# Performance work log

Measured on AMD Instinct MI355X. Metric: run time of the kernel, lower is better.

## Reference

```python
import jax, jax.numpy as jnp
import numpy as np

K1, K2 = 3, 3
DIL = 1
PAD = (DIL * (K1 - 1) // 2, DIL * (K2 - 1) // 2)


def _unfold(x, k1, k2, dilation, padding):
    # x: [B, C, H, W] -> patches [B, C, k1*k2, H*W], matching F.unfold ordering
    B, C, H, W = x.shape
    p0, p1 = padding
    xp = jnp.pad(x, ((0, 0), (0, 0), (p0, p0), (p1, p1)))
    cols = []
    for i in range(k1):  # small fixed loop over kernel taps
        for j in range(k2):
            cols.append(xp[:, :, i * dilation:i * dilation + H, j * dilation:j * dilation + W])
    patches = jnp.stack(cols, axis=2)  # [B, C, k1*k2, H, W]
    return patches.reshape(B, C, k1 * k2, H * W)


def setup_inputs() -> dict:
    key = jax.random.key(0)
    k1, k2, k3, k4 = jax.random.split(key, 4)
    B, Cin, Cout, H, W = 32, 128, 128, 32, 32
    x = jax.random.normal(k1, (B, Cin, H, W), dtype=jnp.float32)
    mask = jax.random.uniform(k2, (1, K1 * K2, H * W), dtype=jnp.float32)
    weight = jax.random.normal(k3, (Cout, Cin, K1, K2), dtype=jnp.float32) * 0.05
    bias = jax.random.normal(k4, (Cout,), dtype=jnp.float32) * 0.05
    return {"x": x, "mask": mask, "weight": weight, "bias": bias}


def reference(x, mask, weight, bias):
    B, Cin, H, W = x.shape
    Cout = weight.shape[0]
    KK = K1 * K2
    # unfold -> [B, Cin, KK, L]
    patches = _unfold(x, K1, K2, DIL, PAD)
    # per-patch mask multiply (mask broadcasts over B and Cin): mask [1, KK, L]
    patches = patches * mask[:, None, :, :]  # [B, Cin, KK, L]
    # dense matmul with flattened weight [Cout, Cin*KK]
    wm = weight.reshape(Cout, Cin * KK)
    out = jnp.einsum('ok,bkl->bol', wm, patches.reshape(B, Cin * KK, H * W))
    out = out + bias[None, :, None]
    return out.reshape(B, Cout, H, W)
```

## Files before the change

kernel.cpp:

```cpp
#include <hip/hip_runtime.h>
#include <hip/hip_fp16.h>

typedef _Float16 half8 __attribute__((ext_vector_type(8)));
typedef float f32x4 __attribute__((ext_vector_type(4)));

#define CIN   128
#define COUT  128
#define HH    32
#define WW    32
#define LTOT  1024
#define KKT   9
#define KDIM  1152

#define SMEM_BYTES 69632

__global__ void prep_w_kernel(const float* __restrict__ w, _Float16* __restrict__ wt) {
  int i = blockIdx.x * 256 + threadIdx.x;
  int q = i >> 10;
  int o = (i >> 3) & 127;
  int j = i & 7;
  int kk = q >> 4;
  int c  = ((q & 15) << 3) + j;
  wt[i] = (_Float16)w[(o * CIN + c) * KKT + kk];
}

__global__ __launch_bounds__(512, 2)
void conv_mfma_kernel(const float* __restrict__ x,
                      const _Float16* __restrict__ wt,
                      const float* __restrict__ mask,
                      const float* __restrict__ bias,
                      float* __restrict__ out) {
  extern __shared__ char smem[];
  const int tid = threadIdx.x;
  int bid = blockIdx.x;
  bid = (bid & 7) * 32 + (bid >> 3);
  const int b  = bid >> 3;
  const int l0 = (bid & 7) << 7;
  const int h0 = (bid & 7) << 2;

  const int lane = tid & 63, wid = tid >> 6;
  const int lr = lane & 15, lg = lane >> 4;
  const int kh = wid >> 2;
  const int wq = wid & 3;
  const int mw = (wq >> 1) << 6;
  const int nw = (wq & 1) << 6;

  float mv[9][4];
  {
    const float* mr = mask + l0 + nw + lr;
#pragma unroll
    for (int kk = 0; kk < 9; ++kk)
#pragma unroll
      for (int nj = 0; nj < 4; ++nj)
        mv[kk][nj] = mr[kk * LTOT + nj * 16];
  }

  const int wv = tid & 31, q16 = tid >> 5;
  char* bdst = smem + wv * 256 + ((q16 ^ (wv & 15)) << 4);
  const float* xb = x + (size_t)b * CIN * LTOT;
  {
    float fr[6][8];
#pragma unroll
    for (int r = 0; r < 6; ++r) {
      const int hg = h0 - 1 + r;
      if ((unsigned)hg < (unsigned)HH) {
        const float* s = xb + (size_t)q16 * 8 * LTOT + hg * WW + wv;
#pragma unroll
        for (int j = 0; j < 8; ++j) fr[r][j] = s[(size_t)j * LTOT];
      }
    }
    asm volatile("s_waitcnt vmcnt(0)" ::: "memory");
#pragma unroll
    for (int r = 0; r < 6; ++r) {
      const int hg = h0 - 1 + r;
      half8 v = (half8){0, 0, 0, 0, 0, 0, 0, 0};
      if ((unsigned)hg < (unsigned)HH) {
#pragma unroll
        for (int j = 0; j < 8; ++j) v[j] = (_Float16)fr[r][j];
      }
      *(half8*)(bdst + r * 8192) = v;
    }
  }
#pragma unroll
  for (int kk = 0; kk < 9; ++kk)
#pragma unroll
    for (int nj = 0; nj < 4; ++nj)
      asm volatile("" : "+v"(mv[kk][nj]));
  __syncthreads();

  const char* abase = (const char*)wt + lg * 2048 + (mw + lr) * 16;

  f32x4 acc[4][4];
#pragma unroll
  for (int mi = 0; mi < 4; ++mi)
#pragma unroll
    for (int nj = 0; nj < 4; ++nj)
      acc[mi][nj] = (f32x4){0.f, 0.f, 0.f, 0.f};

#pragma unroll
  for (int kk = 0; kk < 9; ++kk) {
    const int di = (kk * 11) >> 5;
    const int dj = kk - 3 * di;

    const char* Bp[4];
    int xk[4];
    _Float16 mh[4];
#pragma unroll
    for (int nj = 0; nj < 4; ++nj) {
      const int wb = ((nj & 1) << 4) + lr + dj - 1;
      const bool vld = (unsigned)wb < (unsigned)WW;
      const int wc = vld ? wb : 0;
      const int hrow = (nw >> 5) + (nj >> 1) + di;
      Bp[nj] = smem + hrow * 8192 + wc * 256;
      xk[nj] = wc & 15;
      mh[nj] = (_Float16)(vld ? mv[kk][nj] : 0.f);
    }

    __builtin_amdgcn_s_setprio(1);
#pragma unroll
    for (int s = 0; s < 2; ++s) {
      const int qb = kk * 16 + (kh * 2 + s) * 4;
      const char* ab = abase + qb * 2048;
      const int q = qb + lg;
      half8 a0 = *(const half8*)(ab);
      half8 a1 = *(const half8*)(ab + 256);
      half8 a2 = *(const half8*)(ab + 512);
      half8 a3 = *(const half8*)(ab + 768);
      half8 b0 = *(const half8*)(Bp[0] + (((q & 15) ^ xk[0]) << 4)) * mh[0];
      half8 b1 = *(const half8*)(Bp[1] + (((q & 15) ^ xk[1]) << 4)) * mh[1];
      half8 b2 = *(const half8*)(Bp[2] + (((q & 15) ^ xk[2]) << 4)) * mh[2];
      half8 b3 = *(const half8*)(Bp[3] + (((q & 15) ^ xk[3]) << 4)) * mh[3];
      acc[0][0] = __builtin_amdgcn_mfma_f32_16x16x32_f16(a0, b0, acc[0][0], 0, 0, 0);
      acc[1][0] = __builtin_amdgcn_mfma_f32_16x16x32_f16(a1, b0, acc[1][0], 0, 0, 0);
      acc[2][0] = __builtin_amdgcn_mfma_f32_16x16x32_f16(a2, b0, acc[2][0], 0, 0, 0);
      acc[3][0] = __builtin_amdgcn_mfma_f32_16x16x32_f16(a3, b0, acc[3][0], 0, 0, 0);
      acc[0][1] = __builtin_amdgcn_mfma_f32_16x16x32_f16(a0, b1, acc[0][1], 0, 0, 0);
      acc[1][1] = __builtin_amdgcn_mfma_f32_16x16x32_f16(a1, b1, acc[1][1], 0, 0, 0);
      acc[2][1] = __builtin_amdgcn_mfma_f32_16x16x32_f16(a2, b1, acc[2][1], 0, 0, 0);
      acc[3][1] = __builtin_amdgcn_mfma_f32_16x16x32_f16(a3, b1, acc[3][1], 0, 0, 0);
      acc[0][2] = __builtin_amdgcn_mfma_f32_16x16x32_f16(a0, b2, acc[0][2], 0, 0, 0);
      acc[1][2] = __builtin_amdgcn_mfma_f32_16x16x32_f16(a1, b2, acc[1][2], 0, 0, 0);
      acc[2][2] = __builtin_amdgcn_mfma_f32_16x16x32_f16(a2, b2, acc[2][2], 0, 0, 0);
      acc[3][2] = __builtin_amdgcn_mfma_f32_16x16x32_f16(a3, b2, acc[3][2], 0, 0, 0);
      acc[0][3] = __builtin_amdgcn_mfma_f32_16x16x32_f16(a0, b3, acc[0][3], 0, 0, 0);
      acc[1][3] = __builtin_amdgcn_mfma_f32_16x16x32_f16(a1, b3, acc[1][3], 0, 0, 0);
      acc[2][3] = __builtin_amdgcn_mfma_f32_16x16x32_f16(a2, b3, acc[2][3], 0, 0, 0);
      acc[3][3] = __builtin_amdgcn_mfma_f32_16x16x32_f16(a3, b3, acc[3][3], 0, 0, 0);
    }
    __builtin_amdgcn_s_setprio(0);
  }

  __syncthreads();
  char* red = smem + wq * 17408 + lane * 272;
  if (kh == 1) {
#pragma unroll
    for (int mi = 0; mi < 4; ++mi)
#pragma unroll
      for (int nj = 0; nj < 4; ++nj)
        *(f32x4*)(red + (mi * 4 + nj) * 16) = acc[mi][nj];
  }
  __syncthreads();

  if (kh == 0) {
#pragma unroll
    for (int mi = 0; mi < 4; ++mi)
#pragma unroll
      for (int nj = 0; nj < 4; ++nj) {
        f32x4 p = *(const f32x4*)(red + (mi * 4 + nj) * 16);
        acc[mi][nj].x += p.x; acc[mi][nj].y += p.y;
        acc[mi][nj].z += p.z; acc[mi][nj].w += p.w;
      }

    float* outb = out + (size_t)b * COUT * LTOT + l0;
#pragma unroll
    for (int mi = 0; mi < 4; ++mi) {
#pragma unroll
      for (int rr = 0; rr < 4; ++rr) {
        const int o = mw + mi * 16 + lg * 4 + rr;
        const float bv = bias[o];
        float* orow = outb + (size_t)o * LTOT + nw + lr;
#pragma unroll
        for (int nj = 0; nj < 4; ++nj)
          orow[nj * 16] = acc[mi][nj][rr] + bv;
      }
    }
  }
}

extern "C" void kernel_launch(void* const* d_in, const int* in_sizes, int n_in,
                              void* d_out, int out_size, void* d_ws, size_t ws_size,
                              hipStream_t stream) {
  const float* x    = (const float*)d_in[0];
  const float* mask = (const float*)d_in[1];
  const float* w    = (const float*)d_in[2];
  const float* bias = (const float*)d_in[3];
  float* out = (float*)d_out;
  _Float16* wt = (_Float16*)d_ws;

  (void)hipFuncSetAttribute(reinterpret_cast<const void*>(conv_mfma_kernel),
                            hipFuncAttributeMaxDynamicSharedMemorySize, SMEM_BYTES);

  prep_w_kernel<<<576, 256, 0, stream>>>(w, wt);
  conv_mfma_kernel<<<256, 512, SMEM_BYTES, stream>>>(x, wt, mask, bias, out);
}
```

Baseline: 26.06 us.

## Software-pipeline weight loads two steps ahead and pack mask as fp16

Restructures the main loop into 18 flat steps and prefetches the global weight fragments two steps ahead into registers, so global load latency overlaps with the MFMA work. Mask values are held as packed fp16 instead of fp32 to save registers. Launch bounds drop to one block per CU, which allows more registers per thread for the prefetch buffers. The cost is lower occupancy, so fewer waves are available to hide latency.

```diff
diff --git a/kernel.cpp b/kernel.cpp
--- a/kernel.cpp
+++ b/kernel.cpp
@@ -2,6 +2,7 @@
 #include <hip/hip_fp16.h>
 
 typedef _Float16 half8 __attribute__((ext_vector_type(8)));
+typedef _Float16 half4 __attribute__((ext_vector_type(4)));
 typedef float f32x4 __attribute__((ext_vector_type(4)));
 
 #define CIN   128
@@ -24,7 +25,7 @@
   wt[i] = (_Float16)w[(o * CIN + c) * KKT + kk];
 }
 
-__global__ __launch_bounds__(512, 2)
+__global__ __launch_bounds__(512, 1)
 void conv_mfma_kernel(const float* __restrict__ x,
                       const _Float16* __restrict__ wt,
                       const float* __restrict__ mask,
@@ -45,14 +46,14 @@
   const int mw = (wq >> 1) << 6;
   const int nw = (wq & 1) << 6;
 
-  float mv[9][4];
+  half4 mvh[9];
   {
     const float* mr = mask + l0 + nw + lr;
 #pragma unroll
-    for (int kk = 0; kk < 9; ++kk)
-#pragma unroll
-      for (int nj = 0; nj < 4; ++nj)
-        mv[kk][nj] = mr[kk * LTOT + nj * 16];
+    for (int kk = 0; kk < 9; ++kk) {
+#pragma unroll
+      for (int nj = 0; nj < 4; ++nj) mvh[kk][nj] = (_Float16)mr[kk * LTOT + nj * 16];
+    }
   }
 
   const int wv = tid & 31, q16 = tid >> 5;
@@ -81,11 +82,6 @@
       *(half8*)(bdst + r * 8192) = v;
     }
   }
-#pragma unroll
-  for (int kk = 0; kk < 9; ++kk)
-#pragma unroll
-    for (int nj = 0; nj < 4; ++nj)
-      asm volatile("" : "+v"(mv[kk][nj]));
   __syncthreads();
 
   const char* abase = (const char*)wt + lg * 2048 + (mw + lr) * 16;
@@ -97,56 +93,58 @@
     for (int nj = 0; nj < 4; ++nj)
       acc[mi][nj] = (f32x4){0.f, 0.f, 0.f, 0.f};
 
-#pragma unroll
-  for (int kk = 0; kk < 9; ++kk) {
+  half8 apf[20][4];
+  auto loadA = [&](int s) {
+    const int kk = s >> 1, hs = s & 1;
+    const int qb = kk * 16 + (kh * 2 + hs) * 4;
+    const char* ab = abase + qb * 2048;
+    apf[s][0] = *(const half8*)(ab);
+    apf[s][1] = *(const half8*)(ab + 256);
+    apf[s][2] = *(const half8*)(ab + 512);
+    apf[s][3] = *(const half8*)(ab + 768);
+  };
+  loadA(0);
+  loadA(1);
+
+#pragma unroll
+  for (int s = 0; s < 18; ++s) {
+    if (s + 2 < 18) loadA(s + 2);
+
+    const int kk = s >> 1, hs = s & 1;
     const int di = (kk * 11) >> 5;
     const int dj = kk - 3 * di;
-
-    const char* Bp[4];
-    int xk[4];
-    _Float16 mh[4];
+    const int qb = kk * 16 + (kh * 2 + hs) * 4;
+    const int q15 = (qb + lg) & 15;
+
+    half8 bfr[4];
 #pragma unroll
     for (int nj = 0; nj < 4; ++nj) {
       const int wb = ((nj & 1) << 4) + lr + dj - 1;
       const bool vld = (unsigned)wb < (unsigned)WW;
       const int wc = vld ? wb : 0;
       const int hrow = (nw >> 5) + (nj >> 1) + di;
-      Bp[nj] = smem + hrow * 8192 + wc * 256;
-      xk[nj] = wc & 15;
-      mh[nj] = (_Float16)(vld ? mv[kk][nj] : 0.f);
+      const _Float16 mh = vld ? mvh[kk][nj] : (_Float16)0.f;
+      bfr[nj] = *(const half8*)(smem + hrow * 8192 + wc * 256 +
+                                ((q15 ^ (wc & 15)) << 4)) * mh;
     }
 
     __builtin_amdgcn_s_setprio(1);
-#pragma unroll
-    for (int s = 0; s < 2; ++s) {
-      const int qb = kk * 16 + (kh * 2 + s) * 4;
-      const char* ab = abase + qb * 2048;
-      const int q = qb + lg;
-      half8 a0 = *(const half8*)(ab);
-      half8 a1 = *(const half8*)(ab + 256);
-      half8 a2 = *(const half8*)(ab + 512);
-      half8 a3 = *(const half8*)(ab + 768);
-      half8 b0 = *(const half8*)(Bp[0] + (((q & 15) ^ xk[0]) << 4)) * mh[0];
-      half8 b1 = *(const half8*)(Bp[1] + (((q & 15) ^ xk[1]) << 4)) * mh[1];
-      half8 b2 = *(const half8*)(Bp[2] + (((q & 15) ^ xk[2]) << 4)) * mh[2];
-      half8 b3 = *(const half8*)(Bp[3] + (((q & 15) ^ xk[3]) << 4)) * mh[3];
-      acc[0][0] = __builtin_amdgcn_mfma_f32_16x16x32_f16(a0, b0, acc[0][0], 0, 0, 0);
-      acc[1][0] = __builtin_amdgcn_mfma_f32_16x16x32_f16(a1, b0, acc[1][0], 0, 0, 0);
-      acc[2][0] = __builtin_amdgcn_mfma_f32_16x16x32_f16(a2, b0, acc[2][0], 0, 0, 0);
-      acc[3][0] = __builtin_amdgcn_mfma_f32_16x16x32_f16(a3, b0, acc[3][0], 0, 0, 0);
-      acc[0][1] = __builtin_amdgcn_mfma_f32_16x16x32_f16(a0, b1, acc[0][1], 0, 0, 0);
-      acc[1][1] = __builtin_amdgcn_mfma_f32_16x16x32_f16(a1, b1, acc[1][1], 0, 0, 0);
-      acc[2][1] = __builtin_amdgcn_mfma_f32_16x16x32_f16(a2, b1, acc[2][1], 0, 0, 0);
-      acc[3][1] = __builtin_amdgcn_mfma_f32_16x16x32_f16(a3, b1, acc[3][1], 0, 0, 0);
-      acc[0][2] = __builtin_amdgcn_mfma_f32_16x16x32_f16(a0, b2, acc[0][2], 0, 0, 0);
-      acc[1][2] = __builtin_amdgcn_mfma_f32_16x16x32_f16(a1, b2, acc[1][2], 0, 0, 0);
-      acc[2][2] = __builtin_amdgcn_mfma_f32_16x16x32_f16(a2, b2, acc[2][2], 0, 0, 0);
-      acc[3][2] = __builtin_amdgcn_mfma_f32_16x16x32_f16(a3, b2, acc[3][2], 0, 0, 0);
-      acc[0][3] = __builtin_amdgcn_mfma_f32_16x16x32_f16(a0, b3, acc[0][3], 0, 0, 0);
-      acc[1][3] = __builtin_amdgcn_mfma_f32_16x16x32_f16(a1, b3, acc[1][3], 0, 0, 0);
-      acc[2][3] = __builtin_amdgcn_mfma_f32_16x16x32_f16(a2, b3, acc[2][3], 0, 0, 0);
-      acc[3][3] = __builtin_amdgcn_mfma_f32_16x16x32_f16(a3, b3, acc[3][3], 0, 0, 0);
-    }
+    acc[0][0] = __builtin_amdgcn_mfma_f32_16x16x32_f16(apf[s][0], bfr[0], acc[0][0], 0, 0, 0);
+    acc[1][0] = __builtin_amdgcn_mfma_f32_16x16x32_f16(apf[s][1], bfr[0], acc[1][0], 0, 0, 0);
+    acc[2][0] = __builtin_amdgcn_mfma_f32_16x16x32_f16(apf[s][2], bfr[0], acc[2][0], 0, 0, 0);
+    acc[3][0] = __builtin_amdgcn_mfma_f32_16x16x32_f16(apf[s][3], bfr[0], acc[3][0], 0, 0, 0);
+    acc[0][1] = __builtin_amdgcn_mfma_f32_16x16x32_f16(apf[s][0], bfr[1], acc[0][1], 0, 0, 0);
+    acc[1][1] = __builtin_amdgcn_mfma_f32_16x16x32_f16(apf[s][1], bfr[1], acc[1][1], 0, 0, 0);
+    acc[2][1] = __builtin_amdgcn_mfma_f32_16x16x32_f16(apf[s][2], bfr[1], acc[2][1], 0, 0, 0);
+    acc[3][1] = __builtin_amdgcn_mfma_f32_16x16x32_f16(apf[s][3], bfr[1], acc[3][1], 0, 0, 0);
+    acc[0][2] = __builtin_amdgcn_mfma_f32_16x16x32_f16(apf[s][0], bfr[2], acc[0][2], 0, 0, 0);
+    acc[1][2] = __builtin_amdgcn_mfma_f32_16x16x32_f16(apf[s][1], bfr[2], acc[1][2], 0, 0, 0);
+    acc[2][2] = __builtin_amdgcn_mfma_f32_16x16x32_f16(apf[s][2], bfr[2], acc[2][2], 0, 0, 0);
+    acc[3][2] = __builtin_amdgcn_mfma_f32_16x16x32_f16(apf[s][3], bfr[2], acc[3][2], 0, 0, 0);
+    acc[0][3] = __builtin_amdgcn_mfma_f32_16x16x32_f16(apf[s][0], bfr[3], acc[0][3], 0, 0, 0);
+    acc[1][3] = __builtin_amdgcn_mfma_f32_16x16x32_f16(apf[s][1], bfr[3], acc[1][3], 0, 0, 0);
+    acc[2][3] = __builtin_amdgcn_mfma_f32_16x16x32_f16(apf[s][2], bfr[3], acc[2][3], 0, 0, 0);
+    acc[3][3] = __builtin_amdgcn_mfma_f32_16x16x32_f16(apf[s][3], bfr[3], acc[3][3], 0, 0, 0);
     __builtin_amdgcn_s_setprio(0);
   }
 
```

Result: slower. 27.16 us (+4.2%).

## Prefetch weight fragments one tap ahead and split split-K reduction across both wave halves

Applied to the files above, without the earlier changes.

Weight A-fragments are now held in registers and loaded for the next kernel tap while the current tap's MFMAs run. The first tap's weights are issued alongside the x staging loads, so global latency on weights overlaps compute instead of stalling each step. The mask is kept as packed half4 registers to free VGPRs. The epilogue reduction now has both K-halves exchange half of their accumulators, so all eight waves add and store rows instead of only four. Register pressure rises from the extra prefetch buffers, which may affect occupancy at launch bounds (512,2).

```diff
diff --git a/kernel.cpp b/kernel.cpp
--- a/kernel.cpp
+++ b/kernel.cpp
@@ -2,6 +2,7 @@
 #include <hip/hip_fp16.h>
 
 typedef _Float16 half8 __attribute__((ext_vector_type(8)));
+typedef _Float16 half4 __attribute__((ext_vector_type(4)));
 typedef float f32x4 __attribute__((ext_vector_type(4)));
 
 #define CIN   128
@@ -45,50 +46,62 @@
   const int mw = (wq >> 1) << 6;
   const int nw = (wq & 1) << 6;
 
-  float mv[9][4];
+  half4 mvh[9];
   {
     const float* mr = mask + l0 + nw + lr;
 #pragma unroll
     for (int kk = 0; kk < 9; ++kk)
 #pragma unroll
       for (int nj = 0; nj < 4; ++nj)
-        mv[kk][nj] = mr[kk * LTOT + nj * 16];
+        mvh[kk][nj] = (_Float16)mr[kk * LTOT + nj * 16];
   }
 
   const int wv = tid & 31, q16 = tid >> 5;
   char* bdst = smem + wv * 256 + ((q16 ^ (wv & 15)) << 4);
   const float* xb = x + (size_t)b * CIN * LTOT;
-  {
-    float fr[6][8];
-#pragma unroll
-    for (int r = 0; r < 6; ++r) {
-      const int hg = h0 - 1 + r;
-      if ((unsigned)hg < (unsigned)HH) {
-        const float* s = xb + (size_t)q16 * 8 * LTOT + hg * WW + wv;
-#pragma unroll
-        for (int j = 0; j < 8; ++j) fr[r][j] = s[(size_t)j * LTOT];
-      }
-    }
-    asm volatile("s_waitcnt vmcnt(0)" ::: "memory");
-#pragma unroll
-    for (int r = 0; r < 6; ++r) {
-      const int hg = h0 - 1 + r;
-      half8 v = (half8){0, 0, 0, 0, 0, 0, 0, 0};
-      if ((unsigned)hg < (unsigned)HH) {
-#pragma unroll
-        for (int j = 0; j < 8; ++j) v[j] = (_Float16)fr[r][j];
-      }
-      *(half8*)(bdst + r * 8192) = v;
-    }
-  }
-#pragma unroll
-  for (int kk = 0; kk < 9; ++kk)
-#pragma unroll
-    for (int nj = 0; nj < 4; ++nj)
-      asm volatile("" : "+v"(mv[kk][nj]));
+  float fr[6][8];
+#pragma unroll
+  for (int r = 0; r < 6; ++r) {
+    const int hg = h0 - 1 + r;
+    if ((unsigned)hg < (unsigned)HH) {
+      const float* s = xb + (size_t)q16 * 8 * LTOT + hg * WW + wv;
+#pragma unroll
+      for (int j = 0; j < 8; ++j) fr[r][j] = s[(size_t)j * LTOT];
+    }
+  }
+
+  const char* abase = (const char*)wt + lg * 2048 + (mw + lr) * 16;
+  const char* abE = abase + (kh * 8) * 2048;
+  const char* abO = abase + (kh * 8 + 4) * 2048;
+  half8 aE0 = *(const half8*)(abE);
+  half8 aE1 = *(const half8*)(abE + 256);
+  half8 aE2 = *(const half8*)(abE + 512);
+  half8 aE3 = *(const half8*)(abE + 768);
+  half8 aO0 = *(const half8*)(abO);
+  half8 aO1 = *(const half8*)(abO + 256);
+  half8 aO2 = *(const half8*)(abO + 512);
+  half8 aO3 = *(const half8*)(abO + 768);
+
+  asm volatile("s_waitcnt vmcnt(0)" ::: "memory");
+  asm volatile("" : "+v"(aE0), "+v"(aE1), "+v"(aE2), "+v"(aE3));
+  asm volatile("" : "+v"(aO0), "+v"(aO1), "+v"(aO2), "+v"(aO3));
+#pragma unroll
+  for (int kk = 0; kk < 9; ++kk) asm volatile("" : "+v"(mvh[kk]));
+
+#pragma unroll
+  for (int r = 0; r < 6; ++r) {
+    const int hg = h0 - 1 + r;
+    half8 v = (half8){0, 0, 0, 0, 0, 0, 0, 0};
+    if ((unsigned)hg < (unsigned)HH) {
+#pragma unroll
+      for (int j = 0; j < 8; ++j) v[j] = (_Float16)fr[r][j];
+    }
+    *(half8*)(bdst + r * 8192) = v;
+  }
   __syncthreads();
 
-  const char* abase = (const char*)wt + lg * 2048 + (mw + lr) * 16;
+  const int cE = kh * 8 + lg;
+  const int cO = cE + 4;
 
   f32x4 acc[4][4];
 #pragma unroll
@@ -113,75 +126,108 @@
       const int hrow = (nw >> 5) + (nj >> 1) + di;
       Bp[nj] = smem + hrow * 8192 + wc * 256;
       xk[nj] = wc & 15;
-      mh[nj] = (_Float16)(vld ? mv[kk][nj] : 0.f);
-    }
-
-    __builtin_amdgcn_s_setprio(1);
-#pragma unroll
-    for (int s = 0; s < 2; ++s) {
-      const int qb = kk * 16 + (kh * 2 + s) * 4;
-      const char* ab = abase + qb * 2048;
-      const int q = qb + lg;
-      half8 a0 = *(const half8*)(ab);
-      half8 a1 = *(const half8*)(ab + 256);
-      half8 a2 = *(const half8*)(ab + 512);
-      half8 a3 = *(const half8*)(ab + 768);
-      half8 b0 = *(const half8*)(Bp[0] + (((q & 15) ^ xk[0]) << 4)) * mh[0];
-      half8 b1 = *(const half8*)(Bp[1] + (((q & 15) ^ xk[1]) << 4)) * mh[1];
-      half8 b2 = *(const half8*)(Bp[2] + (((q & 15) ^ xk[2]) << 4)) * mh[2];
-      half8 b3 = *(const half8*)(Bp[3] + (((q & 15) ^ xk[3]) << 4)) * mh[3];
-      acc[0][0] = __builtin_amdgcn_mfma_f32_16x16x32_f16(a0, b0, acc[0][0], 0, 0, 0);
-      acc[1][0] = __builtin_amdgcn_mfma_f32_16x16x32_f16(a1, b0, acc[1][0], 0, 0, 0);
-      acc[2][0] = __builtin_amdgcn_mfma_f32_16x16x32_f16(a2, b0, acc[2][0], 0, 0, 0);
-      acc[3][0] = __builtin_amdgcn_mfma_f32_16x16x32_f16(a3, b0, acc[3][0], 0, 0, 0);
-      acc[0][1] = __builtin_amdgcn_mfma_f32_16x16x32_f16(a0, b1, acc[0][1], 0, 0, 0);
-      acc[1][1] = __builtin_amdgcn_mfma_f32_16x16x32_f16(a1, b1, acc[1][1], 0, 0, 0);
-      acc[2][1] = __builtin_amdgcn_mfma_f32_16x16x32_f16(a2, b1, acc[2][1], 0, 0, 0);
-      acc[3][1] = __builtin_amdgcn_mfma_f32_16x16x32_f16(a3, b1, acc[3][1], 0, 0, 0);
-      acc[0][2] = __builtin_amdgcn_mfma_f32_16x16x32_f16(a0, b2, acc[0][2], 0, 0, 0);
-      acc[1][2] = __builtin_amdgcn_mfma_f32_16x16x32_f16(a1, b2, acc[1][2], 0, 0, 0);
-      acc[2][2] = __builtin_amdgcn_mfma_f32_16x16x32_f16(a2, b2, acc[2][2], 0, 0, 0);
-      acc[3][2] = __builtin_amdgcn_mfma_f32_16x16x32_f16(a3, b2, acc[3][2], 0, 0, 0);
-      acc[0][3] = __builtin_amdgcn_mfma_f32_16x16x32_f16(a0, b3, acc[0][3], 0, 0, 0);
-      acc[1][3] = __builtin_amdgcn_mfma_f32_16x16x32_f16(a1, b3, acc[1][3], 0, 0, 0);
-      acc[2][3] = __builtin_amdgcn_mfma_f32_16x16x32_f16(a2, b3, acc[2][3], 0, 0, 0);
-      acc[3][3] = __builtin_amdgcn_mfma_f32_16x16x32_f16(a3, b3, acc[3][3], 0, 0, 0);
-    }
-    __builtin_amdgcn_s_setprio(0);
+      mh[nj] = vld ? mvh[kk][nj] : (_Float16)0.f;
+    }
+
+    {
+      half8 b0 = *(const half8*)(Bp[0] + ((cE ^ xk[0]) << 4)) * mh[0];
+      half8 b1 = *(const half8*)(Bp[1] + ((cE ^ xk[1]) << 4)) * mh[1];
+      half8 b2 = *(const half8*)(Bp[2] + ((cE ^ xk[2]) << 4)) * mh[2];
+      half8 b3 = *(const half8*)(Bp[3] + ((cE ^ xk[3]) << 4)) * mh[3];
+      __builtin_amdgcn_s_setprio(1);
+      acc[0][0] = __builtin_amdgcn_mfma_f32_16x16x32_f16(aE0, b0, acc[0][0], 0, 0, 0);
+      acc[1][0] = __builtin_amdgcn_mfma_f32_16x16x32_f16(aE1, b0, acc[1][0], 0, 0, 0);
+      acc[2][0] = __builtin_amdgcn_mfma_f32_16x16x32_f16(aE2, b0, acc[2][0], 0, 0, 0);
+      acc[3][0] = __builtin_amdgcn_mfma_f32_16x16x32_f16(aE3, b0, acc[3][0], 0, 0, 0);
+      acc[0][1] = __builtin_amdgcn_mfma_f32_16x16x32_f16(aE0, b1, acc[0][1], 0, 0, 0);
+      acc[1][1] = __builtin_amdgcn_mfma_f32_16x16x32_f16(aE1, b1, acc[1][1], 0, 0, 0);
+      acc[2][1] = __builtin_amdgcn_mfma_f32_16x16x32_f16(aE2, b1, acc[2][1], 0, 0, 0);
+      acc[3][1] = __builtin_amdgcn_mfma_f32_16x16x32_f16(aE3, b1, acc[3][1], 0, 0, 0);
+      acc[0][2] = __builtin_amdgcn_mfma_f32_16x16x32_f16(aE0, b2, acc[0][2], 0, 0, 0);
+      acc[1][2] = __builtin_amdgcn_mfma_f32_16x16x32_f16(aE1, b2, acc[1][2], 0, 0, 0);
+      acc[2][2] = __builtin_amdgcn_mfma_f32_16x16x32_f16(aE2, b2, acc[2][2], 0, 0, 0);
+      acc[3][2] = __builtin_amdgcn_mfma_f32_16x16x32_f16(aE3, b2, acc[3][2], 0, 0, 0);
+      acc[0][3] = __builtin_amdgcn_mfma_f32_16x16x32_f16(aE0, b3, acc[0][3], 0, 0, 0);
+      acc[1][3] = __builtin_amdgcn_mfma_f32_16x16x32_f16(aE1, b3, acc[1][3], 0, 0, 0);
+      acc[2][3] = __builtin_amdgcn_mfma_f32_16x16x32_f16(aE2, b3, acc[2][3], 0, 0, 0);
+      acc[3][3] = __builtin_amdgcn_mfma_f32_16x16x32_f16(aE3, b3, acc[3][3], 0, 0, 0);
+      __builtin_amdgcn_s_setprio(0);
+      if (kk < 8) {
+        const char* ne = abase + ((kk + 1) * 16 + kh * 8) * 2048;
+        aE0 = *(const half8*)(ne);
+        aE1 = *(const half8*)(ne + 256);
+        aE2 = *(const half8*)(ne + 512);
+        aE3 = *(const half8*)(ne + 768);
+      }
+    }
+
+    {
+      half8 b0 = *(const half8*)(Bp[0] + ((cO ^ xk[0]) << 4)) * mh[0];
+      half8 b1 = *(const half8*)(Bp[1] + ((cO ^ xk[1]) << 4)) * mh[1];
+      half8 b2 = *(const half8*)(Bp[2] + ((cO ^ xk[2]) << 4)) * mh[2];
+      half8 b3 = *(const half8*)(Bp[3] + ((cO ^ xk[3]) << 4)) * mh[3];
+      __builtin_amdgcn_s_setprio(1);
+      acc[0][0] = __builtin_amdgcn_mfma_f32_16x16x32_f16(aO0, b0, acc[0][0], 0, 0, 0);
+      acc[1][0] = __builtin_amdgcn_mfma_f32_16x16x32_f16(aO1, b0, acc[1][0], 0, 0, 0);
+      acc[2][0] = __builtin_amdgcn_mfma_f32_16x16x32_f16(aO2, b0, acc[2][0], 0, 0, 0);
+      acc[3][0] = __builtin_amdgcn_mfma_f32_16x16x32_f16(aO3, b0, acc[3][0], 0, 0, 0);
+      acc[0][1] = __builtin_amdgcn_mfma_f32_16x16x32_f16(aO0, b1, acc[0][1], 0, 0, 0);
+      acc[1][1] = __builtin_amdgcn_mfma_f32_16x16x32_f16(aO1, b1, acc[1][1], 0, 0, 0);
+      acc[2][1] = __builtin_amdgcn_mfma_f32_16x16x32_f16(aO2, b1, acc[2][1], 0, 0, 0);
+      acc[3][1] = __builtin_amdgcn_mfma_f32_16x16x32_f16(aO3, b1, acc[3][1], 0, 0, 0);
+      acc[0][2] = __builtin_amdgcn_mfma_f32_16x16x32_f16(aO0, b2, acc[0][2], 0, 0, 0);
+      acc[1][2] = __builtin_amdgcn_mfma_f32_16x16x32_f16(aO1, b2, acc[1][2], 0, 0, 0);
+      acc[2][2] = __builtin_amdgcn_mfma_f32_16x16x32_f16(aO2, b2, acc[2][2], 0, 0, 0);
+      acc[3][2] = __builtin_amdgcn_mfma_f32_16x16x32_f16(aO3, b2, acc[3][2], 0, 0, 0);
+      acc[0][3] = __builtin_amdgcn_mfma_f32_16x16x32_f16(aO0, b3, acc[0][3], 0, 0, 0);
+      acc[1][3] = __builtin_amdgcn_mfma_f32_16x16x32_f16(aO1, b3, acc[1][3], 0, 0, 0);
+      acc[2][3] = __builtin_amdgcn_mfma_f32_16x16x32_f16(aO2, b3, acc[2][3], 0, 0, 0);
+      acc[3][3] = __builtin_amdgcn_mfma_f32_16x16x32_f16(aO3, b3, acc[3][3], 0, 0, 0);
+      __builtin_amdgcn_s_setprio(0);
+      if (kk < 8) {
+        const char* no_ = abase + ((kk + 1) * 16 + kh * 8 + 4) * 2048;
+        aO0 = *(const half8*)(no_);
+        aO1 = *(const half8*)(no_ + 256);
+        aO2 = *(const half8*)(no_ + 512);
+        aO3 = *(const half8*)(no_ + 768);
+      }
+    }
   }
 
   __syncthreads();
-  char* red = smem + wq * 17408 + lane * 272;
-  if (kh == 1) {
-#pragma unroll
-    for (int mi = 0; mi < 4; ++mi)
+  {
+    char* myred = smem + wid * 8192 + lane * 128;
+    const int miW = (kh == 0) ? 2 : 0;
+#pragma unroll
+    for (int m2 = 0; m2 < 2; ++m2)
 #pragma unroll
       for (int nj = 0; nj < 4; ++nj)
-        *(f32x4*)(red + (mi * 4 + nj) * 16) = acc[mi][nj];
+        *(f32x4*)(myred + (m2 * 4 + nj) * 16) = acc[miW + m2][nj];
   }
   __syncthreads();
-
-  if (kh == 0) {
-#pragma unroll
-    for (int mi = 0; mi < 4; ++mi)
+  {
+    const char* pred = smem + (wid ^ 4) * 8192 + lane * 128;
+    const int miS = (kh == 0) ? 0 : 2;
+    float* outb = out + (size_t)b * COUT * LTOT + l0;
+#pragma unroll
+    for (int m2 = 0; m2 < 2; ++m2) {
+      f32x4 sum[4];
 #pragma unroll
       for (int nj = 0; nj < 4; ++nj) {
-        f32x4 p = *(const f32x4*)(red + (mi * 4 + nj) * 16);
-        acc[mi][nj].x += p.x; acc[mi][nj].y += p.y;
-        acc[mi][nj].z += p.z; acc[mi][nj].w += p.w;
-      }
-
-    float* outb = out + (size_t)b * COUT * LTOT + l0;
-#pragma unroll
-    for (int mi = 0; mi < 4; ++mi) {
+        f32x4 p = *(const f32x4*)(pred + (m2 * 4 + nj) * 16);
+        sum[nj].x = acc[miS + m2][nj].x + p.x;
+        sum[nj].y = acc[miS + m2][nj].y + p.y;
+        sum[nj].z = acc[miS + m2][nj].z + p.z;
+        sum[nj].w = acc[miS + m2][nj].w + p.w;
+      }
 #pragma unroll
       for (int rr = 0; rr < 4; ++rr) {
-        const int o = mw + mi * 16 + lg * 4 + rr;
+        const int o = mw + (miS + m2) * 16 + lg * 4 + rr;
         const float bv = bias[o];
         float* orow = outb + (size_t)o * LTOT + nw + lr;
 #pragma unroll
         for (int nj = 0; nj < 4; ++nj)
-          orow[nj * 16] = acc[mi][nj][rr] + bv;
+          orow[nj * 16] = sum[nj][rr] + bv;
       }
     }
   }
```

New measurement: 25.80 us. No clear change (-1.0%).
